# Optimization experiments

Hardware: AMD Instinct MI355X
Metric: run time of the kernel (lower is better)

Reference implementation:

```python
import jax, jax.numpy as jnp
import numpy as np

B, L, K, D = 1, 4096, 24, 512


def setup_inputs() -> dict:
    key = jax.random.key(0)
    k1, k2, k3, k4 = jax.random.split(key, 4)
    u = jax.random.normal(k1, (B, L, D), dtype=jnp.float32)
    # spectral filter bank (learned parameter initialized from Hankel eigenvectors in the
    # original; random init is equivalent for a correctness baseline), scaled ~O(1/sqrt(L))
    filters = jax.random.normal(k2, (L, K), dtype=jnp.float32) * (1.0 / np.sqrt(L))
    M_phi_plus = jax.random.normal(k3, (K, D, D), dtype=jnp.float32) * (1.0 / np.sqrt(K * D))
    M_phi_minus = jax.random.normal(k4, (K, D, D), dtype=jnp.float32) * (1.0 / np.sqrt(K * D))
    return {"u": u, "filters": filters, "M_phi_plus": M_phi_plus, "M_phi_minus": M_phi_minus}


def _causal_conv(u, phi):
    # Causal linear convolution of every input channel with every spectral filter via FFT.
    # u: [B, L, D], phi: [L, K] -> [B, L, K, D]
    L_ = u.shape[1]
    n = 2 * L_  # zero-pad so circular FFT conv == linear causal conv
    Uf = jnp.fft.rfft(u, n=n, axis=1)                    # [B, F, D]
    Pf = jnp.fft.rfft(phi, n=n, axis=0)                  # [F, K]
    prod = Uf[:, :, None, :] * Pf[None, :, :, None]      # [B, F, K, D]
    return jnp.fft.irfft(prod, n=n, axis=1)[:, :L_]      # [B, L, K, D]


def reference(u, filters, M_phi_plus, M_phi_minus):
    L_ = u.shape[1]
    # sgn[t] = (-1)^t ; U_minus[b,l,k,d] = sum_s u[b,s,d] * phi[l-s,k] * (-1)^(l-s),
    # which equals convolving with the alternating-sign filter phi[t]*(-1)^t
    # (the original implements this as sgn-pre/post-multiplication around FlashFFTConv).
    sgn = jnp.where(jnp.arange(L_) % 2 == 0, 1.0, -1.0).astype(u.dtype)
    U_plus = _causal_conv(u, filters)                      # [B, L, K, D]
    U_minus = _causal_conv(u, filters * sgn[:, None])      # [B, L, K, D]
    y = (jnp.einsum('blkd,kdo->blo', U_plus, M_phi_plus)
         + jnp.einsum('blkd,kdo->blo', U_minus, M_phi_minus))
    return y
```

## Files before the change

kernel.cpp:

```cpp
#include <hip/hip_runtime.h>
#include <hip/hip_bf16.h>
#include <cstdint>
#include <cstddef>

using bf16 = __hip_bfloat16;

typedef __attribute__((ext_vector_type(4))) float f32x4;
typedef __attribute__((ext_vector_type(8))) short s16x8;

#define LSEQ 4096
#define DDIM 512
#define KFLT 24
#define NFFT 8192
#define MR 8192

__device__ __forceinline__ void gld16(const bf16* g, bf16* l) {
  __builtin_amdgcn_global_load_lds((const __attribute__((address_space(1))) void*)g,
                                   (__attribute__((address_space(3))) void*)l, 16, 0, 0);
}

#define MEMFENCE asm volatile("" ::: "memory")
#define BAR() do { MEMFENCE; __builtin_amdgcn_s_barrier(); MEMFENCE; } while (0)

__device__ __forceinline__ float fsin_rev(float rev) {
  float s; asm("v_sin_f32 %0, %1" : "=v"(s) : "v"(rev)); return s;
}
__device__ __forceinline__ float fcos_rev(float rev) {
  float c; asm("v_cos_f32 %0, %1" : "=v"(c) : "v"(rev)); return c;
}

__device__ __forceinline__ void stage_half(const bf16* g, int ldk, bf16* ldsbase,
                                           int wave, int lane) {
  const int r8 = lane >> 3;
  const int sc = ((lane & 7) ^ r8) * 8;
  #pragma unroll
  for (int q = 0; q < 2; ++q) {
    const int c = wave * 2 + q;
    gld16(g + (size_t)(c * 8 + r8) * ldk + sc, ldsbase + c * 512);
  }
}

__device__ __forceinline__ s16x8 ldfrag(const bf16* buf, int row, int kk, int l4) {
  return *(const s16x8*)(buf + row * 64 + (((kk * 4 + l4) ^ (row & 7)) * 8));
}

__global__ __launch_bounds__(256) void transpose_cast(
    const float* __restrict__ in, bf16* __restrict__ out, int R, int C) {
  __shared__ float tile[32][33];
  const size_t bo = (size_t)blockIdx.z * R * C;
  const float* inb = in + bo;
  bf16* outb = out + bo;
  int c0 = blockIdx.x * 32, r0 = blockIdx.y * 32;
  int tx = threadIdx.x & 31, ty = threadIdx.x >> 5;
  #pragma unroll
  for (int i = 0; i < 32; i += 8)
    tile[ty + i][tx] = inb[(size_t)(r0 + ty + i) * C + (c0 + tx)];
  __syncthreads();
  #pragma unroll
  for (int i = 0; i < 32; i += 8)
    outb[(size_t)(c0 + ty + i) * R + (r0 + tx)] = __float2bfloat16(tile[tx][ty + i]);
}

__global__ __launch_bounds__(256) void add2_cast(
    const bf16* __restrict__ P, bf16* __restrict__ out) {
  size_t i = ((size_t)blockIdx.x * 256 + threadIdx.x) * 8;
  const size_t MN = (size_t)MR * DDIM;
  s16x8 a = *(const s16x8*)(P + i);
  s16x8 b = *(const s16x8*)(P + i + MN);
  bf16 o[8];
  #pragma unroll
  for (int e = 0; e < 8; ++e) {
    float fa = __uint_as_float((unsigned)(unsigned short)a[e] << 16);
    float fb = __uint_as_float((unsigned)(unsigned short)b[e] << 16);
    o[e] = __float2bfloat16(fa + fb);
  }
  *(s16x8*)(out + i) = *(const s16x8*)o;
}

__global__ __launch_bounds__(256) void tr_reduce4(
    const float* __restrict__ S, bf16* __restrict__ out) {
  __shared__ float tile[32][33];
  int c0 = blockIdx.x * 32, r0 = blockIdx.y * 32;
  int tx = threadIdx.x & 31, ty = threadIdx.x >> 5;
  const int nt = c0 >> 8;
  const int scl = (c0 & 255) + tx;
  const size_t SB = (size_t)MR * 256;
  #pragma unroll
  for (int i = 0; i < 32; i += 8) {
    size_t ro = (size_t)(r0 + ty + i) * 256 + scl;
    tile[ty + i][tx] = S[(0 * 2 + nt) * SB + ro] + S[(1 * 2 + nt) * SB + ro] +
                       S[(2 * 2 + nt) * SB + ro] + S[(3 * 2 + nt) * SB + ro];
  }
  __syncthreads();
  #pragma unroll
  for (int i = 0; i < 32; i += 8)
    out[(size_t)(c0 + ty + i) * MR + (r0 + tx)] = __float2bfloat16(tile[tx][ty + i]);
}

__global__ __launch_bounds__(256) void reduce4y(
    const float* __restrict__ P, const float* __restrict__ vnyq,
    float* __restrict__ y) {
  size_t i = ((size_t)blockIdx.x * 256 + threadIdx.x) * 4;
  const size_t MN = (size_t)LSEQ * DDIM;
  int l = (int)(i >> 9), o = (int)(i & 511);
  f32x4 a = *(const f32x4*)(P + i);
  f32x4 b = *(const f32x4*)(P + i + MN);
  f32x4 c = *(const f32x4*)(P + i + 2 * MN);
  f32x4 d = *(const f32x4*)(P + i + 3 * MN);
  f32x4 v = *(const f32x4*)(vnyq + o);
  float sg = (l & 1) ? -(1.f / NFFT) : (1.f / NFFT);
  f32x4 r = a + b + c + d;
  r[0] += sg * v[0]; r[1] += sg * v[1]; r[2] += sg * v[2]; r[3] += sg * v[3];
  *(f32x4*)(y + i) = r;
}

__global__ __launch_bounds__(256) void compute_pf(
    const float* __restrict__ phi, float* __restrict__ Pf) {
  int f0 = blockIdx.x * 2;
  int tid = threadIdx.x;
  int lane = tid & 63, wave = tid >> 6;
  float pre[2][KFLT], pim[2][KFLT];
  #pragma unroll
  for (int ff = 0; ff < 2; ++ff)
    #pragma unroll
    for (int k = 0; k < KFLT; ++k) { pre[ff][k] = 0.f; pim[ff][k] = 0.f; }
  for (int cch = 0; cch < LSEQ / 256; ++cch) {
    int t = cch * 256 + tid;
    const float4* pv = (const float4*)(phi + (size_t)t * KFLT);
    float4 v0 = pv[0], v1 = pv[1], v2 = pv[2], v3 = pv[3], v4 = pv[4], v5 = pv[5];
    float pr[KFLT] = {v0.x, v0.y, v0.z, v0.w, v1.x, v1.y, v1.z, v1.w,
                      v2.x, v2.y, v2.z, v2.w, v3.x, v3.y, v3.z, v3.w,
                      v4.x, v4.y, v4.z, v4.w, v5.x, v5.y, v5.z, v5.w};
    #pragma unroll
    for (int ff = 0; ff < 2; ++ff) {
      int m = ((f0 + ff) * t) & (NFFT - 1);
      float rev = (float)m * (1.f / NFFT);
      float s = fsin_rev(rev), c = fcos_rev(rev);
      #pragma unroll
      for (int k = 0; k < KFLT; ++k) {
        pre[ff][k] += pr[k] * c;
        pim[ff][k] -= pr[k] * s;
      }
    }
  }
  __shared__ float red[4][2][2 * KFLT];
  #pragma unroll
  for (int ff = 0; ff < 2; ++ff)
    #pragma unroll
    for (int k = 0; k < KFLT; ++k) {
      float r = pre[ff][k], i2 = pim[ff][k];
      #pragma unroll
      for (int off = 32; off > 0; off >>= 1) {
        r += __shfl_down(r, off, 64);
        i2 += __shfl_down(i2, off, 64);
      }
      if (lane == 0) { red[wave][ff][2 * k] = r; red[wave][ff][2 * k + 1] = i2; }
    }
  __syncthreads();
  if (tid < 96) {
    int ff = tid / 48, q = tid % 48;
    int f = f0 + ff;
    if (f <= NFFT / 2)
      Pf[(size_t)f * 48 + q] =
          red[0][ff][q] + red[1][ff][q] + red[2][ff][q] + red[3][ff][q];
  }
}

__global__ __launch_bounds__(256) void build_pw(
    const float* __restrict__ Pf, float* __restrict__ Pw, float* __restrict__ wnyq) {
  int idx = blockIdx.x * 256 + threadIdx.x;
  int j = idx >> 12, f = idx & 4095;
  float re, im;
  if (j < KFLT) {
    re = Pf[(size_t)f * 48 + j * 2];
    im = Pf[(size_t)f * 48 + j * 2 + 1];
  } else {
    int k = j - KFLT, g = NFFT / 2 - f;
    re = Pf[(size_t)g * 48 + k * 2];
    im = -Pf[(size_t)g * 48 + k * 2 + 1];
  }
  Pw[(size_t)idx * 2] = re;
  Pw[(size_t)idx * 2 + 1] = im;
  if (idx < 48)
    wnyq[idx] = (idx < KFLT) ? Pf[(size_t)(NFFT / 2) * 48 + idx * 2]
                             : Pf[(idx - KFLT) * 2];
}

__global__ __launch_bounds__(256) void nyq_u(
    const float* __restrict__ u, float* __restrict__ Unyq) {
  int d = blockIdx.x * 256 + threadIdx.x;
  int t0 = blockIdx.y * 64;
  float acc = 0.f;
  for (int t = t0; t < t0 + 64; t += 2)
    acc += u[(size_t)t * DDIM + d] - u[(size_t)(t + 1) * DDIM + d];
  atomicAdd(&Unyq[d], acc);
}

__global__ __launch_bounds__(256) void vnyq_k(
    const bf16* __restrict__ Mt, const float* __restrict__ Unyq,
    const float* __restrict__ wnyq, float* __restrict__ vnyq) {
  __shared__ float us[DDIM];
  int j = blockIdx.x, tid = threadIdx.x;
  us[tid] = Unyq[tid];
  us[tid + 256] = Unyq[tid + 256];
  __syncthreads();
  float w = wnyq[j];
  int o = blockIdx.y * 128 + (tid >> 1);
  int dh = (tid & 1) * 256;
  const bf16* row = Mt + ((size_t)j * DDIM + o) * DDIM + dh;
  float acc = 0.f;
  for (int d0 = 0; d0 < 256; d0 += 8) {
    s16x8 v = *(const s16x8*)(row + d0);
    #pragma unroll
    for (int e = 0; e < 8; ++e)
      acc += us[dh + d0 + e] * __uint_as_float((unsigned)(unsigned short)v[e] << 16);
  }
  acc += __shfl_xor(acc, 1, 64);
  if ((tid & 1) == 0) atomicAdd(&vnyq[o], w * acc);
}

template <int STORE>
__global__ __launch_bounds__(512, 2) void gemmG(
    const bf16* __restrict__ Bt, int ldk,
    bf16* __restrict__ Obf, float* __restrict__ Of) {
  __shared__ bf16 sA[3 * 128 * 64];
  __shared__ bf16 sB[3 * 256 * 64];

  const int lin = blockIdx.x;
  const int wid = (lin & 7) * 32 + (lin >> 3);

  int mt, nt, kt0, nkt, ks;
  if constexpr (STORE == 0) {
    ks = wid >> 7; int rem = wid & 127; mt = rem >> 1; nt = rem & 1;
    kt0 = ks * 32; nkt = 32;
  } else {
    ks = wid >> 6; int rem = wid & 63; mt = rem >> 1; nt = rem & 1;
    kt0 = ks * 32; nkt = 32;
  }

  const int tid = threadIdx.x, lane = tid & 63, wave = tid >> 6;
  const int l15 = lane & 15, l4 = lane >> 4;
  const int wr = wave >> 2, wc = wave & 3;
  const int r8 = lane >> 3, c8 = lane & 7;
  const int mtile = mt * 128, ntile = nt * 256;
  const bf16* Bb = Bt + (size_t)ntile * ldk;

  f32x4 acc[4][4];
  #pragma unroll
  for (int m = 0; m < 4; ++m)
    #pragma unroll
    for (int n = 0; n < 4; ++n) acc[m][n] = f32x4{0.f, 0.f, 0.f, 0.f};

  auto genA = [&](int t, int buf) {
    const int kbase = (kt0 + t) * 64 + ((c8 ^ r8) * 8);
    #pragma unroll
    for (int q = 0; q < 2; ++q) {
      const int c = wave * 2 + q;
      const int row = mtile + c * 8 + r8;
      bf16 o[8];
      if constexpr (STORE == 0) {
        const int f = row >> 1;
        const bool odd = row & 1;
        #pragma unroll
        for (int e = 0; e < 8; ++e) {
          int m = (f * (kbase + e)) & (NFFT - 1);
          float rev = (float)m * (1.f / NFFT);
          o[e] = __float2bfloat16(odd ? -fsin_rev(rev) : fcos_rev(rev));
        }
      } else {
        #pragma unroll
        for (int e = 0; e < 8; ++e) {
          int r = kbase + e;
          int f = r >> 1;
          int m = (f * row) & (NFFT - 1);
          float rev = (float)m * (1.f / NFFT);
          float sc2 = ((f == 0) ? 1.f : 2.f) * (1.f / NFFT);
          o[e] = __float2bfloat16((r & 1) ? -sc2 * fsin_rev(rev)
                                          : sc2 * fcos_rev(rev));
        }
      }
      *(s16x8*)(sA + buf * (128 * 64) + (c * 8 + r8) * 64 + c8 * 8) =
          *(const s16x8*)o;
    }
  };
  auto stageB = [&](int t, int buf) {
    const size_t ko = (size_t)(kt0 + t) * 64;
    stage_half(Bb + ko, ldk, sB + buf * (256 * 64), wave, lane);
    stage_half(Bb + (size_t)128 * ldk + ko, ldk, sB + buf * (256 * 64) + 128 * 64,
               wave, lane);
  };

  genA(0, 0);
  genA(1, 1);
  stageB(0, 0);
  stageB(1, 1);
  asm volatile("s_waitcnt vmcnt(4)" ::: "memory");
  asm volatile("s_waitcnt lgkmcnt(0)" ::: "memory");
  BAR();

  for (int t = 0; t < nkt; ++t) {
    const int buf = t % 3;
    const bf16* bA = sA + buf * (128 * 64);
    const bf16* bB = sB + buf * (256 * 64);
    const bool i2 = (t + 2 < nkt);

    s16x8 afr[4][2], bfr[4][2];
    #pragma unroll
    for (int n = 0; n < 4; ++n)
      #pragma unroll
      for (int kk = 0; kk < 2; ++kk)
        bfr[n][kk] = ldfrag(bB, wc * 64 + n * 16 + l15, kk, l4);
    #pragma unroll
    for (int m = 0; m < 4; ++m)
      #pragma unroll
      for (int kk = 0; kk < 2; ++kk)
        afr[m][kk] = ldfrag(bA, wr * 64 + m * 16 + l15, kk, l4);

    if (i2) {
      genA(t + 2, (t + 2) % 3);
      stageB(t + 2, (t + 2) % 3);
    }

    __builtin_amdgcn_s_setprio(1);
    #pragma unroll
    for (int m = 0; m < 4; ++m)
      #pragma unroll
      for (int n = 0; n < 4; ++n)
        #pragma unroll
        for (int kk = 0; kk < 2; ++kk)
          acc[m][n] = __builtin_amdgcn_mfma_f32_16x16x32_bf16(
              afr[m][kk], bfr[n][kk], acc[m][n], 0, 0, 0);
    __builtin_amdgcn_s_setprio(0);

    if (i2) { asm volatile("s_waitcnt vmcnt(4)" ::: "memory"); }
    else    { asm volatile("s_waitcnt vmcnt(0)" ::: "memory"); }
    asm volatile("s_waitcnt lgkmcnt(0)" ::: "memory");
    BAR();
  }

  #pragma unroll
  for (int m = 0; m < 4; ++m)
    #pragma unroll
    for (int n = 0; n < 4; ++n)
      #pragma unroll
      for (int e = 0; e < 4; ++e) {
        int row = mtile + wr * 64 + m * 16 + l4 * 4 + e;
        int col = ntile + wc * 64 + n * 16 + l15;
        if constexpr (STORE == 0)
          Obf[(size_t)ks * MR * DDIM + (size_t)row * DDIM + col] =
              __float2bfloat16(acc[m][n][e]);
        else
          Of[(size_t)ks * LSEQ * DDIM + (size_t)row * DDIM + col] = acc[m][n][e];
      }
}

struct ARegs { int4 a[4]; float2 w[2]; };

__global__ __launch_bounds__(512, 2) void gemmW(
    const bf16* __restrict__ Auf, const bf16* __restrict__ Mt,
    const float* __restrict__ Pw, float* __restrict__ Slots) {
  __shared__ bf16 sA[2 * 256 * 64];
  __shared__ bf16 sB[3 * 256 * 64];

  const int lin = blockIdx.x;
  const int q = lin & 7;
  const int pos = lin >> 3;
  const int jg = q >> 1, mhalf = q & 1;
  const int nt = pos >> 4;
  const int mt = mhalf * 16 + (pos & 15);

  const int tid = threadIdx.x, lane = tid & 63, wave = tid >> 6;
  const int l15 = lane & 15, l4 = lane >> 4;
  const int wr = wave >> 2, wc = wave & 3;
  const int r8 = lane >> 3, c8 = lane & 7;

  float* dst = Slots + (size_t)(jg * 2 + nt) * ((size_t)MR * 256);

  f32x4 acc[8][4];
  #pragma unroll
  for (int m = 0; m < 8; ++m)
    #pragma unroll
    for (int n = 0; n < 4; ++n) acc[m][n] = f32x4{0.f, 0.f, 0.f, 0.f};

  auto J  = [&](int s) { return jg * 12 + (s >> 3); };
  auto KT = [&](int s) { return s & 7; };

  auto issueA = [&](int j, int kt, ARegs& r) {
    #pragma unroll
    for (int qq = 0; qq < 2; ++qq) {
      int row_e = wave * 32 + 2 * (qq * 8 + r8);
      int rg = mt * 256 + row_e;
      const bf16* p = Auf + (size_t)rg * DDIM + kt * 64 + c8 * 8;
      r.a[2 * qq]     = *(const int4*)p;
      r.a[2 * qq + 1] = *(const int4*)(p + DDIM);
      r.w[qq] = *(const float2*)(Pw + ((size_t)j * 4096 + (rg >> 1)) * 2);
    }
  };
  auto writeA = [&](bf16* db, const ARegs& r) {
    #pragma unroll
    for (int qq = 0; qq < 2; ++qq) {
      int row_e = wave * 32 + 2 * (qq * 8 + r8);
      union { int4 i; unsigned short u[8]; } ae, ao;
      ae.i = r.a[2 * qq]; ao.i = r.a[2 * qq + 1];
      bf16 oe[8], oo[8];
      #pragma unroll
      for (int e = 0; e < 8; ++e) {
        float fe = __uint_as_float((unsigned)ae.u[e] << 16);
        float fo = __uint_as_float((unsigned)ao.u[e] << 16);
        oe[e] = __float2bfloat16(r.w[qq].x * fe - r.w[qq].y * fo);
        oo[e] = __float2bfloat16(r.w[qq].x * fo + r.w[qq].y * fe);
      }
      *(s16x8*)(db + row_e * 64 + ((c8 ^ (row_e & 7)) * 8)) = *(const s16x8*)oe;
      *(s16x8*)(db + (row_e + 1) * 64 + ((c8 ^ ((row_e + 1) & 7)) * 8)) =
          *(const s16x8*)oo;
    }
  };
  auto stageB = [&](int j, int kt, bf16* db) {
    const bf16* bb = Mt + (size_t)j * (DDIM * DDIM) + (size_t)(nt * 256) * DDIM + kt * 64;
    stage_half(bb, DDIM, db, wave, lane);
    stage_half(bb + (size_t)128 * DDIM, DDIM, db + 128 * 64, wave, lane);
  };

  ARegs rA, rB_;

  {
    ARegs t0;
    issueA(J(0), KT(0), t0);
    stageB(J(0), KT(0), sB);
    asm volatile("s_waitcnt vmcnt(4)" ::: "memory");
    writeA(sA, t0);
    issueA(J(1), KT(1), rA);
    stageB(J(1), KT(1), sB + 256 * 64);
    asm volatile("s_waitcnt vmcnt(10)" ::: "memory");
    asm volatile("s_waitcnt lgkmcnt(0)" ::: "memory");
    BAR();
  }

  auto unit = [&](int s, ARegs& cur, ARegs& nxt) {
    const bf16* bA = sA + (s & 1) * (256 * 64);
    const bf16* bB = sB + (s % 3) * (256 * 64);
    const bool i2 = (s + 2 < 96);

    s16x8 bfr[4][2], afr[4][2];
    #pragma unroll
    for (int n = 0; n < 4; ++n)
      #pragma unroll
      for (int kk = 0; kk < 2; ++kk)
        bfr[n][kk] = ldfrag(bB, wc * 64 + n * 16 + l15, kk, l4);
    #pragma unroll
    for (int m = 0; m < 4; ++m)
      #pragma unroll
      for (int kk = 0; kk < 2; ++kk)
        afr[m][kk] = ldfrag(bA, wr * 128 + m * 16 + l15, kk, l4);

    if (i2) {
      issueA(J(s + 2), KT(s + 2), nxt);
      stageB(J(s + 2), KT(s + 2), sB + ((s + 2) % 3) * (256 * 64));
    }

    __builtin_amdgcn_s_setprio(1);
    #pragma unroll
    for (int m = 0; m < 4; ++m)
      #pragma unroll
      for (int n = 0; n < 4; ++n)
        #pragma unroll
        for (int kk = 0; kk < 2; ++kk)
          acc[m][n] = __builtin_amdgcn_mfma_f32_16x16x32_bf16(
              afr[m][kk], bfr[n][kk], acc[m][n], 0, 0, 0);
    __builtin_amdgcn_s_setprio(0);

    #pragma unroll
    for (int m = 0; m < 4; ++m)
      #pragma unroll
      for (int kk = 0; kk < 2; ++kk)
        afr[m][kk] = ldfrag(bA, wr * 128 + 64 + m * 16 + l15, kk, l4);

    if (s + 1 < 96) {
      if (i2) { asm volatile("s_waitcnt vmcnt(10)" ::: "memory"); }
      else    { asm volatile("s_waitcnt vmcnt(0)" ::: "memory"); }
      writeA(sA + ((s + 1) & 1) * (256 * 64), cur);
    }

    __builtin_amdgcn_s_setprio(1);
    #pragma unroll
    for (int m = 0; m < 4; ++m)
      #pragma unroll
      for (int n = 0; n < 4; ++n)
        #pragma unroll
        for (int kk = 0; kk < 2; ++kk)
          acc[4 + m][n] = __builtin_amdgcn_mfma_f32_16x16x32_bf16(
              afr[m][kk], bfr[n][kk], acc[4 + m][n], 0, 0, 0);
    __builtin_amdgcn_s_setprio(0);

    asm volatile("s_waitcnt lgkmcnt(0)" ::: "memory");
    BAR();
  };

  for (int sp = 0; sp < 48; ++sp) {
    unit(2 * sp,     rA, rB_);
    unit(2 * sp + 1, rB_, rA);
  }

  #pragma unroll
  for (int m = 0; m < 8; ++m)
    #pragma unroll
    for (int n = 0; n < 4; ++n)
      #pragma unroll
      for (int e = 0; e < 4; ++e) {
        int row = mt * 256 + wr * 128 + (m & 3) * 16 + (m >> 2) * 64 + l4 * 4 + e;
        int col = wc * 64 + n * 16 + l15;
        dst[(size_t)row * 256 + col] = acc[m][n][e];
      }
}

#define WS_W     0ULL
#define WS_AUF   67108864ULL
#define WS_UT    75497472ULL
#define WS_MT    79691776ULL
#define WS_PF    104857600ULL
#define WS_PW    105644288ULL
#define WS_WNYQ  107217152ULL
#define WS_UNYQ  107217408ULL
#define WS_VNYQ  107219456ULL
#define WS_YBT   107221504ULL
#define WS_G1P   115610112ULL
#define WS_TOTAL 132387328ULL

extern "C" void kernel_launch(void* const* d_in, const int* in_sizes, int n_in,
                              void* d_out, int out_size, void* d_ws, size_t ws_size,
                              hipStream_t stream) {
  const float* u   = (const float*)d_in[0];
  const float* phi = (const float*)d_in[1];
  const float* Mp  = (const float*)d_in[2];
  const float* Mm  = (const float*)d_in[3];
  float* y = (float*)d_out;

  if (ws_size < WS_TOTAL) return;

  char* ws = (char*)d_ws;
  float* Slots= (float*)(ws + WS_W);
  bf16*  Auf  = (bf16*)(ws + WS_AUF);
  bf16*  uT   = (bf16*)(ws + WS_UT);
  bf16*  Mt   = (bf16*)(ws + WS_MT);
  float* Pf   = (float*)(ws + WS_PF);
  float* Pw   = (float*)(ws + WS_PW);
  float* wny  = (float*)(ws + WS_WNYQ);
  float* Uny  = (float*)(ws + WS_UNYQ);
  float* vny  = (float*)(ws + WS_VNYQ);
  bf16*  Ybt  = (bf16*)(ws + WS_YBT);
  bf16*  G1P  = (bf16*)(ws + WS_G1P);
  float* G3P  = (float*)(ws + WS_AUF);

  transpose_cast<<<dim3(16, 128, 1), 256, 0, stream>>>(u, uT, LSEQ, DDIM);
  transpose_cast<<<dim3(16, 16, 24), 256, 0, stream>>>(Mp, Mt, DDIM, DDIM);
  transpose_cast<<<dim3(16, 16, 24), 256, 0, stream>>>(Mm, Mt + (size_t)24 * DDIM * DDIM,
                                                       DDIM, DDIM);
  compute_pf<<<dim3(2049), 256, 0, stream>>>(phi, Pf);
  build_pw<<<dim3(48 * 4096 / 256), 256, 0, stream>>>(Pf, Pw, wny);
  hipMemsetAsync(Uny, 0, DDIM * sizeof(float), stream);
  nyq_u<<<dim3(2, 64), 256, 0, stream>>>(u, Uny);

  gemmG<0><<<256, 512, 0, stream>>>(uT, LSEQ, G1P, nullptr);
  add2_cast<<<dim3(MR * DDIM / 2048), 256, 0, stream>>>(G1P, Auf);

  gemmW<<<256, 512, 0, stream>>>(Auf, Mt, Pw, Slots);

  tr_reduce4<<<dim3(16, 256), 256, 0, stream>>>(Slots, Ybt);
  hipMemsetAsync(vny, 0, DDIM * sizeof(float), stream);
  vnyq_k<<<dim3(48, 4), 256, 0, stream>>>(Mt, Uny, wny, vny);

  gemmG<1><<<256, 512, 0, stream>>>(Ybt, MR, nullptr, G3P);
  reduce4y<<<dim3(LSEQ * DDIM / 1024), 256, 0, stream>>>(G3P, vny, y);
}
```

Measured before the change: 488.8 us.

## Reuse A tile across filters and apply twiddle in registers via DPP

The gemmW loop is reordered so the filter index runs innermost. Each 64-wide K slice of the A operand is staged into LDS once per kt and held in registers across all 12 filters, instead of being reloaded and re-twiddled from global memory on every step. The complex twiddle multiply now runs in registers just before the MFMAs, using a DPP lane swap to pair even and odd rows, with the twiddle factors preloaded into LDS. The wave layout becomes 4x2 with 64x128 tiles per wave. This cuts global A traffic and the LDS A double buffer, but adds per-step VALU conversion work between MFMA groups, which may compete with matrix throughput.

Measured after the change: 506.5 us. 3.6% more time.

```diff
diff --git a/kernel.cpp b/kernel.cpp
--- a/kernel.cpp
+++ b/kernel.cpp
@@ -354,13 +354,12 @@
       }
 }
 
-struct ARegs { int4 a[4]; float2 w[2]; };
-
 __global__ __launch_bounds__(512, 2) void gemmW(
     const bf16* __restrict__ Auf, const bf16* __restrict__ Mt,
     const float* __restrict__ Pw, float* __restrict__ Slots) {
-  __shared__ bf16 sA[2 * 256 * 64];
   __shared__ bf16 sB[3 * 256 * 64];
+  __shared__ bf16 sA[256 * 64];
+  __shared__ float2 sW[12 * 128];
 
   const int lin = blockIdx.x;
   const int q = lin & 7;
@@ -371,144 +370,120 @@
 
   const int tid = threadIdx.x, lane = tid & 63, wave = tid >> 6;
   const int l15 = lane & 15, l4 = lane >> 4;
-  const int wr = wave >> 2, wc = wave & 3;
-  const int r8 = lane >> 3, c8 = lane & 7;
+  const int wr = wave >> 1, wc = wave & 1;
 
   float* dst = Slots + (size_t)(jg * 2 + nt) * ((size_t)MR * 256);
 
-  f32x4 acc[8][4];
-  #pragma unroll
-  for (int m = 0; m < 8; ++m)
-    #pragma unroll
-    for (int n = 0; n < 4; ++n) acc[m][n] = f32x4{0.f, 0.f, 0.f, 0.f};
-
-  auto J  = [&](int s) { return jg * 12 + (s >> 3); };
-  auto KT = [&](int s) { return s & 7; };
-
-  auto issueA = [&](int j, int kt, ARegs& r) {
-    #pragma unroll
-    for (int qq = 0; qq < 2; ++qq) {
-      int row_e = wave * 32 + 2 * (qq * 8 + r8);
-      int rg = mt * 256 + row_e;
-      const bf16* p = Auf + (size_t)rg * DDIM + kt * 64 + c8 * 8;
-      r.a[2 * qq]     = *(const int4*)p;
-      r.a[2 * qq + 1] = *(const int4*)(p + DDIM);
-      r.w[qq] = *(const float2*)(Pw + ((size_t)j * 4096 + (rg >> 1)) * 2);
-    }
-  };
-  auto writeA = [&](bf16* db, const ARegs& r) {
-    #pragma unroll
-    for (int qq = 0; qq < 2; ++qq) {
-      int row_e = wave * 32 + 2 * (qq * 8 + r8);
-      union { int4 i; unsigned short u[8]; } ae, ao;
-      ae.i = r.a[2 * qq]; ao.i = r.a[2 * qq + 1];
-      bf16 oe[8], oo[8];
-      #pragma unroll
-      for (int e = 0; e < 8; ++e) {
-        float fe = __uint_as_float((unsigned)ae.u[e] << 16);
-        float fo = __uint_as_float((unsigned)ao.u[e] << 16);
-        oe[e] = __float2bfloat16(r.w[qq].x * fe - r.w[qq].y * fo);
-        oo[e] = __float2bfloat16(r.w[qq].x * fo + r.w[qq].y * fe);
-      }
-      *(s16x8*)(db + row_e * 64 + ((c8 ^ (row_e & 7)) * 8)) = *(const s16x8*)oe;
-      *(s16x8*)(db + (row_e + 1) * 64 + ((c8 ^ ((row_e + 1) & 7)) * 8)) =
-          *(const s16x8*)oo;
-    }
-  };
-  auto stageB = [&](int j, int kt, bf16* db) {
+  f32x4 acc[4][8];
+  #pragma unroll
+  for (int m = 0; m < 4; ++m)
+    #pragma unroll
+    for (int n = 0; n < 8; ++n) acc[m][n] = f32x4{0.f, 0.f, 0.f, 0.f};
+
+  auto stageB_ = [&](int s) {
+    const int j = jg * 12 + (s % 12), kt = s / 12;
     const bf16* bb = Mt + (size_t)j * (DDIM * DDIM) + (size_t)(nt * 256) * DDIM + kt * 64;
+    bf16* db = sB + (s % 3) * (256 * 64);
     stage_half(bb, DDIM, db, wave, lane);
     stage_half(bb + (size_t)128 * DDIM, DDIM, db + 128 * 64, wave, lane);
   };
-
-  ARegs rA, rB_;
-
-  {
-    ARegs t0;
-    issueA(J(0), KT(0), t0);
-    stageB(J(0), KT(0), sB);
-    asm volatile("s_waitcnt vmcnt(4)" ::: "memory");
-    writeA(sA, t0);
-    issueA(J(1), KT(1), rA);
-    stageB(J(1), KT(1), sB + 256 * 64);
-    asm volatile("s_waitcnt vmcnt(10)" ::: "memory");
-    asm volatile("s_waitcnt lgkmcnt(0)" ::: "memory");
-    BAR();
-  }
-
-  auto unit = [&](int s, ARegs& cur, ARegs& nxt) {
-    const bf16* bA = sA + (s & 1) * (256 * 64);
+  auto stageA_ = [&](int kt) {
+    const bf16* ab = Auf + (size_t)(mt * 256) * DDIM + kt * 64;
+    stage_half(ab, DDIM, sA, wave, lane);
+    stage_half(ab + (size_t)128 * DDIM, DDIM, sA + 128 * 64, wave, lane);
+  };
+
+  #pragma unroll
+  for (int t = 0; t < 3; ++t) {
+    int idx = tid * 3 + t;
+    int jj2 = idx >> 7, fo = idx & 127;
+    sW[idx] = *(const float2*)(Pw +
+        (((size_t)(jg * 12 + jj2)) * 4096 + (size_t)mt * 128 + fo) * 2);
+  }
+  stageB_(0);
+  stageB_(1);
+  stageA_(0);
+  asm volatile("s_waitcnt vmcnt(0) lgkmcnt(0)" ::: "memory");
+  BAR();
+
+  int4 selfA[4][2];
+
+  for (int s = 0; s < 96; ++s) {
+    const int jj = s % 12, kt = s / 12;
     const bf16* bB = sB + (s % 3) * (256 * 64);
-    const bool i2 = (s + 2 < 96);
-
-    s16x8 bfr[4][2], afr[4][2];
-    #pragma unroll
-    for (int n = 0; n < 4; ++n)
-      #pragma unroll
-      for (int kk = 0; kk < 2; ++kk)
-        bfr[n][kk] = ldfrag(bB, wc * 64 + n * 16 + l15, kk, l4);
-    #pragma unroll
-    for (int m = 0; m < 4; ++m)
-      #pragma unroll
-      for (int kk = 0; kk < 2; ++kk)
-        afr[m][kk] = ldfrag(bA, wr * 128 + m * 16 + l15, kk, l4);
-
-    if (i2) {
-      issueA(J(s + 2), KT(s + 2), nxt);
-      stageB(J(s + 2), KT(s + 2), sB + ((s + 2) % 3) * (256 * 64));
-    }
-
-    __builtin_amdgcn_s_setprio(1);
-    #pragma unroll
-    for (int m = 0; m < 4; ++m)
-      #pragma unroll
-      for (int n = 0; n < 4; ++n)
+
+    if (s) {
+      if (s == 95) { asm volatile("s_waitcnt vmcnt(0)" ::: "memory"); }
+      else         { asm volatile("s_waitcnt vmcnt(4)" ::: "memory"); }
+      BAR();
+    }
+    if (s + 2 < 96) stageB_(s + 2);
+    if (jj == 6 && kt < 7) stageA_(kt + 1);
+
+    if (jj == 0) {
+      #pragma unroll
+      for (int m = 0; m < 4; ++m)
         #pragma unroll
-        for (int kk = 0; kk < 2; ++kk)
+        for (int kk = 0; kk < 2; ++kk) {
+          s16x8 v = ldfrag(sA, wr * 64 + m * 16 + l15, kk, l4);
+          selfA[m][kk] = *(const int4*)&v;
+        }
+    }
+
+    float wx[4], swy[4];
+    #pragma unroll
+    for (int m = 0; m < 4; ++m) {
+      int fr = (wr * 64 + m * 16 + l15) >> 1;
+      float2 w = sW[jj * 128 + fr];
+      wx[m] = w.x;
+      swy[m] = (l15 & 1) ? w.y : -w.y;
+    }
+
+    #pragma unroll
+    for (int kk = 0; kk < 2; ++kk) {
+      s16x8 bfr[8];
+      #pragma unroll
+      for (int n = 0; n < 8; ++n)
+        bfr[n] = ldfrag(bB, wc * 128 + n * 16 + l15, kk, l4);
+      #pragma unroll
+      for (int m = 0; m < 4; ++m) {
+        const int4 sv = selfA[m][kk];
+        int4 pv;
+        pv.x = __builtin_amdgcn_mov_dpp(sv.x, 0xB1, 0xF, 0xF, true);
+        pv.y = __builtin_amdgcn_mov_dpp(sv.y, 0xB1, 0xF, 0xF, true);
+        pv.z = __builtin_amdgcn_mov_dpp(sv.z, 0xB1, 0xF, 0xF, true);
+        pv.w = __builtin_amdgcn_mov_dpp(sv.w, 0xB1, 0xF, 0xF, true);
+        const int sp[4] = {sv.x, sv.y, sv.z, sv.w};
+        const int pp[4] = {pv.x, pv.y, pv.z, pv.w};
+        bf16 ob[8];
+        #pragma unroll
+        for (int t2 = 0; t2 < 4; ++t2) {
+          float fsl = __uint_as_float((unsigned)sp[t2] << 16);
+          float fsh = __uint_as_float((unsigned)sp[t2] & 0xffff0000u);
+          float fpl = __uint_as_float((unsigned)pp[t2] << 16);
+          float fph = __uint_as_float((unsigned)pp[t2] & 0xffff0000u);
+          ob[2 * t2]     = __float2bfloat16(wx[m] * fsl + swy[m] * fpl);
+          ob[2 * t2 + 1] = __float2bfloat16(wx[m] * fsh + swy[m] * fph);
+        }
+        const s16x8 afr = *(const s16x8*)ob;
+        __builtin_amdgcn_s_setprio(1);
+        #pragma unroll
+        for (int n = 0; n < 8; ++n)
           acc[m][n] = __builtin_amdgcn_mfma_f32_16x16x32_bf16(
-              afr[m][kk], bfr[n][kk], acc[m][n], 0, 0, 0);
-    __builtin_amdgcn_s_setprio(0);
-
-    #pragma unroll
-    for (int m = 0; m < 4; ++m)
-      #pragma unroll
-      for (int kk = 0; kk < 2; ++kk)
-        afr[m][kk] = ldfrag(bA, wr * 128 + 64 + m * 16 + l15, kk, l4);
-
-    if (s + 1 < 96) {
-      if (i2) { asm volatile("s_waitcnt vmcnt(10)" ::: "memory"); }
-      else    { asm volatile("s_waitcnt vmcnt(0)" ::: "memory"); }
-      writeA(sA + ((s + 1) & 1) * (256 * 64), cur);
-    }
-
-    __builtin_amdgcn_s_setprio(1);
-    #pragma unroll
-    for (int m = 0; m < 4; ++m)
-      #pragma unroll
-      for (int n = 0; n < 4; ++n)
-        #pragma unroll
-        for (int kk = 0; kk < 2; ++kk)
-          acc[4 + m][n] = __builtin_amdgcn_mfma_f32_16x16x32_bf16(
-              afr[m][kk], bfr[n][kk], acc[4 + m][n], 0, 0, 0);
-    __builtin_amdgcn_s_setprio(0);
-
-    asm volatile("s_waitcnt lgkmcnt(0)" ::: "memory");
-    BAR();
-  };
-
-  for (int sp = 0; sp < 48; ++sp) {
-    unit(2 * sp,     rA, rB_);
-    unit(2 * sp + 1, rB_, rA);
-  }
-
-  #pragma unroll
-  for (int m = 0; m < 8; ++m)
-    #pragma unroll
-    for (int n = 0; n < 4; ++n)
+              afr, bfr[n], acc[m][n], 0, 0, 0);
+        __builtin_amdgcn_s_setprio(0);
+      }
+    }
+  }
+
+  #pragma unroll
+  for (int m = 0; m < 4; ++m)
+    #pragma unroll
+    for (int n = 0; n < 8; ++n)
       #pragma unroll
       for (int e = 0; e < 4; ++e) {
-        int row = mt * 256 + wr * 128 + (m & 3) * 16 + (m >> 2) * 64 + l4 * 4 + e;
-        int col = wc * 64 + n * 16 + l15;
+        int row = mt * 256 + wr * 64 + m * 16 + l4 * 4 + e;
+        int col = wc * 128 + n * 16 + l15;
         dst[(size_t)row * 256 + col] = acc[m][n][e];
       }
 }
```
